# Performance work log

Measured on AMD Instinct MI355X. Metric: run time of the kernel, lower is better.

Reference implementation:

```python
import jax, jax.numpy as jnp
import numpy as np

DIM = 768
HEADS = 12
DIM_HEAD = DIM // HEADS
FACTOR = DIM_HEAD ** (-0.5)
B, T = 4, 2048


def setup_inputs() -> dict:
    key = jax.random.key(0)
    k1, k2, k3 = jax.random.split(key, 3)
    x = jax.random.normal(k1, (B, T, DIM), dtype=jnp.float32)
    # VarianceScaling-like init scale for linear weights
    W_qkv = jax.random.normal(k2, (DIM, 3 * DIM), dtype=jnp.float32) * (DIM ** -0.5)
    W_out = jax.random.normal(k3, (DIM, DIM), dtype=jnp.float32) * (DIM ** -0.5)
    return {"x": x, "W_qkv": W_qkv, "W_out": W_out}


def reference(x, W_qkv, W_out):
    b, t, _ = x.shape
    qkv = x @ W_qkv  # [b, t, 3*dim]
    # einops 'b t (d k h) -> k b h t d' with k=3, h=HEADS: d slowest, k middle, h fastest
    qkv = qkv.reshape(b, t, DIM_HEAD, 3, HEADS)
    qkv = jnp.transpose(qkv, (3, 0, 4, 1, 2))  # [3, b, h, t, d]
    q, k, v = qkv[0], qkv[1], qkv[2]
    # scaled dot-product attention, full [b,h,t,t] scores as in the original
    scores = jnp.einsum('bhid,bhjd->bhij', q, k) * FACTOR
    attn = jax.nn.softmax(scores, axis=-1)
    out = jnp.einsum('bhij,bhjd->bhid', attn, v)  # [b, h, t, d]
    # 'b h t d -> b t (h d)'
    out = jnp.transpose(out, (0, 2, 1, 3)).reshape(b, t, HEADS * DIM_HEAD)
    return out @ W_out
```

## Files before the change

kernel.cpp:

```cpp
#include <hip/hip_runtime.h>
#include <hip/hip_bf16.h>

#define DIM    768
#define HEADS  12
#define DHEAD  64
#define BATCH  4
#define SEQ    2048
#define NROW   (BATCH * SEQ)
#define QKVN   (3 * DIM)
#define FACTOR 0.125f
#define QSCALE 0.18033688011112042f

typedef __attribute__((ext_vector_type(8))) short short8;
typedef __attribute__((ext_vector_type(4))) float floatx4;

__device__ __forceinline__ floatx4 mfma16(short8 a, short8 b, floatx4 c) {
    return __builtin_amdgcn_mfma_f32_16x16x32_bf16(a, b, c, 0, 0, 0);
}

__device__ __forceinline__ short rne16(float f) {
    unsigned u = __builtin_bit_cast(unsigned, f);
    return (short)((u + 0x7fffu + ((u >> 16) & 1u)) >> 16);
}
__device__ __forceinline__ unsigned pack2(float lo, float hi) {
    unsigned ul = __builtin_bit_cast(unsigned, lo);
    unsigned uh = __builtin_bit_cast(unsigned, hi);
    ul = (ul + 0x7fffu + ((ul >> 16) & 1u)) >> 16;
    uh = (uh + 0x7fffu + ((uh >> 16) & 1u)) & 0xffff0000u;
    return ul | uh;
}

__device__ __forceinline__ int swz8(int row, int col) {
    return (row << 6) + ((((col >> 3) ^ row) & 7) << 3) + (col & 7);
}

__global__ __launch_bounds__(256) void conv_bf16(const float* __restrict__ x,
                                                 short* __restrict__ xb) {
    int g = blockIdx.x * 256 + threadIdx.x;
    float4 v = ((const float4*)x)[g];
    uint2 o;
    o.x = pack2(v.x, v.y);
    o.y = pack2(v.z, v.w);
    ((uint2*)xb)[g] = o;
}

__global__ __launch_bounds__(256) void transpose_w(const float* __restrict__ W,
                                                   short* __restrict__ Wt,
                                                   int K, int N, int permute) {
    __shared__ short T[32][33];
    int n0 = blockIdx.x * 32, k0 = blockIdx.y * 32;
    int c = threadIdx.x & 31, r0 = threadIdx.x >> 5;
    for (int r = r0; r < 32; r += 8)
        T[r][c] = rne16(W[(size_t)(k0 + r) * N + n0 + c]);
    __syncthreads();
    for (int r = r0; r < 32; r += 8) {
        int n = n0 + r;
        int np;
        if (permute) {
            int d = n / 36, rem = n - d * 36;
            int which = rem / 12, h = rem - which * 12;
            np = which * 768 + h * 64 + d;
        } else {
            np = n;
        }
        Wt[(size_t)np * K + k0 + c] = T[c][r];
    }
}

__global__ __launch_bounds__(256) void gemm_qkv(const short* __restrict__ A,
                                                const short* __restrict__ Bt,
                                                short* __restrict__ Qo,
                                                short* __restrict__ Ko,
                                                short* __restrict__ Vto) {
    __shared__ short As[128 * 64];
    __shared__ short Bs[128 * 64];
    const int tid = threadIdx.x;
    const int lane = tid & 63, wave = tid >> 6;
    const int l15 = lane & 15, quad = lane >> 4;

    const int flat = blockIdx.x;
    const int xcd = flat & 7;
    const int local = flat >> 3;
    const int mloc = local & 7, nloc = local >> 3;
    const int m0 = (xcd * 8 + mloc) * 128;
    const int n0 = nloc * 128;

    const int wm = (wave >> 1) * 64, wn = (wave & 1) * 64;

    floatx4 acc[4][4] = {};
    for (int k0 = 0; k0 < DIM; k0 += 64) {
#pragma unroll
        for (int i = 0; i < 4; ++i) {
            int idx = tid + i * 256;
            int row = idx >> 3, c = idx & 7;
            int loff = (row << 6) + (((c ^ row) & 7) << 3);
            *(uint4*)&As[loff] = *(const uint4*)&A[(size_t)(m0 + row) * DIM + k0 + c * 8];
            *(uint4*)&Bs[loff] = *(const uint4*)&Bt[(size_t)(n0 + row) * DIM + k0 + c * 8];
        }
        __syncthreads();
#pragma unroll
        for (int ks = 0; ks < 2; ++ks) {
            short8 a[4], b[4];
#pragma unroll
            for (int mt = 0; mt < 4; ++mt)
                a[mt] = *(const short8*)&As[swz8(wm + mt * 16 + l15, ks * 32 + quad * 8)];
#pragma unroll
            for (int nt = 0; nt < 4; ++nt)
                b[nt] = *(const short8*)&Bs[swz8(wn + nt * 16 + l15, ks * 32 + quad * 8)];
#pragma unroll
            for (int mt = 0; mt < 4; ++mt)
#pragma unroll
                for (int nt = 0; nt < 4; ++nt)
                    acc[mt][nt] = mfma16(a[mt], b[nt], acc[mt][nt]);
        }
        __syncthreads();
    }

    const int sn = n0 + wn;
    const int which = sn / 768;
    const int h = (sn - which * 768) >> 6;
    const int bb = (m0 + wm) >> 11;
    const int tbase = (m0 + wm) & 2047;

    if (which != 2) {
        short* dst = (which == 0) ? Qo : Ko;
        const float scale = (which == 0) ? QSCALE : 1.0f;
        const size_t rowbase = ((size_t)(bb * HEADS + h) * SEQ + tbase) * DHEAD;
#pragma unroll
        for (int mt = 0; mt < 4; ++mt)
#pragma unroll
            for (int nt = 0; nt < 4; ++nt) {
                int d = nt * 16 + l15;
#pragma unroll
                for (int r = 0; r < 4; ++r) {
                    int tl = mt * 16 + quad * 4 + r;
                    dst[rowbase + (size_t)tl * DHEAD + d] = rne16(acc[mt][nt][r] * scale);
                }
            }
    } else {
        short* vld = ((wave < 2) ? As : Bs) + (wave & 1) * 4096;
#pragma unroll
        for (int mt = 0; mt < 4; ++mt)
#pragma unroll
            for (int nt = 0; nt < 4; ++nt) {
                int d = nt * 16 + l15;
                int tl = mt * 16 + quad * 4;
                int chunk = (tl >> 3) ^ (d & 7);
                int addr = (d << 6) + (chunk << 3) + (tl & 7);
                uint2 pk;
                pk.x = pack2(acc[mt][nt][0], acc[mt][nt][1]);
                pk.y = pack2(acc[mt][nt][2], acc[mt][nt][3]);
                *(uint2*)&vld[addr] = pk;
            }
    }
    __syncthreads();
    if (which == 2) {
        short* vld = ((wave < 2) ? As : Bs) + (wave & 1) * 4096;
        const size_t vbase = ((size_t)(bb * HEADS + h) * DHEAD) * SEQ;
#pragma unroll
        for (int i = 0; i < 8; ++i) {
            int c = lane + i * 64;
            int d = c >> 3, j = c & 7;
            int addr = (d << 6) + (((j ^ (d & 7)) & 7) << 3);
            uint4 v = *(const uint4*)&vld[addr];
            *(uint4*)&Vto[vbase + (size_t)d * SEQ + tbase + j * 8] = v;
        }
    }
}

__global__ __launch_bounds__(256) void attn_mfma(const short* __restrict__ Q,
                                                 const short* __restrict__ K,
                                                 const short* __restrict__ Vt,
                                                 short* __restrict__ O) {
    __shared__ short Qs[128 * 64];
    __shared__ short Ks[64 * 64];
    __shared__ short Vs[64 * 64];
    __shared__ short Ps[4 * 32 * 64];

    const int tid = threadIdx.x;
    const int lane = tid & 63, wave = tid >> 6;
    const int l15 = lane & 15, quad = lane >> 4;
    const int bh = blockIdx.y;
    const int q0 = blockIdx.x * 128;
    const size_t base = (size_t)bh * SEQ * DHEAD;
    const int wr = wave * 32;
    short* myP = Ps + wave * (32 * 64);

#pragma unroll
    for (int i = 0; i < 4; ++i) {
        int idx = tid + i * 256;
        int row = idx >> 3, c = idx & 7;
        *(uint4*)&Qs[(row << 6) + (((c ^ row) & 7) << 3)] =
            *(const uint4*)&Q[base + (size_t)(q0 + row) * DHEAD + c * 8];
    }

    floatx4 o[2][4] = {};
    float lsum[2] = {0.f, 0.f};

    for (int j0 = 0; j0 < SEQ; j0 += 64) {
#pragma unroll
        for (int i = 0; i < 2; ++i) {
            int idx = tid + i * 256;
            int row = idx >> 3, c = idx & 7;
            int loff = (row << 6) + (((c ^ row) & 7) << 3);
            *(uint4*)&Ks[loff] = *(const uint4*)&K[base + (size_t)(j0 + row) * DHEAD + c * 8];
            *(uint4*)&Vs[loff] = *(const uint4*)&Vt[base + (size_t)row * SEQ + j0 + c * 8];
        }
        __syncthreads();

        floatx4 s[2][4] = {};
#pragma unroll
        for (int ks = 0; ks < 2; ++ks) {
            short8 kf[4], qf[2];
#pragma unroll
            for (int kt = 0; kt < 4; ++kt)
                kf[kt] = *(const short8*)&Ks[swz8(kt * 16 + l15, ks * 32 + quad * 8)];
#pragma unroll
            for (int mt = 0; mt < 2; ++mt)
                qf[mt] = *(const short8*)&Qs[swz8(wr + mt * 16 + l15, ks * 32 + quad * 8)];
#pragma unroll
            for (int mt = 0; mt < 2; ++mt)
#pragma unroll
                for (int kt = 0; kt < 4; ++kt)
                    s[mt][kt] = mfma16(kf[kt], qf[mt], s[mt][kt]);
        }

#pragma unroll
        for (int mt = 0; mt < 2; ++mt)
#pragma unroll
            for (int kt = 0; kt < 4; ++kt) {
                float p0 = __builtin_amdgcn_exp2f(s[mt][kt][0]);
                float p1 = __builtin_amdgcn_exp2f(s[mt][kt][1]);
                float p2 = __builtin_amdgcn_exp2f(s[mt][kt][2]);
                float p3 = __builtin_amdgcn_exp2f(s[mt][kt][3]);
                lsum[mt] += (p0 + p1) + (p2 + p3);
                uint2 pk;
                pk.x = pack2(p0, p1);
                pk.y = pack2(p2, p3);
                *(uint2*)&myP[swz8(mt * 16 + l15, kt * 16 + quad * 4)] = pk;
            }

#pragma unroll
        for (int ks = 0; ks < 2; ++ks) {
            short8 a[2], b[4];
#pragma unroll
            for (int mt = 0; mt < 2; ++mt)
                a[mt] = *(const short8*)&myP[swz8(mt * 16 + l15, ks * 32 + quad * 8)];
#pragma unroll
            for (int dt = 0; dt < 4; ++dt)
                b[dt] = *(const short8*)&Vs[swz8(dt * 16 + l15, ks * 32 + quad * 8)];
#pragma unroll
            for (int mt = 0; mt < 2; ++mt)
#pragma unroll
                for (int dt = 0; dt < 4; ++dt)
                    o[mt][dt] = mfma16(a[mt], b[dt], o[mt][dt]);
        }
        __syncthreads();
    }

    const int b = bh / HEADS, h = bh - b * HEADS;
#pragma unroll
    for (int mt = 0; mt < 2; ++mt) {
        float rs = lsum[mt];
        rs += __shfl_xor(rs, 16);
        rs += __shfl_xor(rs, 32);
        float invl = 1.f / rs;
#pragma unroll
        for (int r = 0; r < 4; ++r) {
            float inv = __shfl(invl, quad * 4 + r);
            int t = q0 + wr + mt * 16 + quad * 4 + r;
#pragma unroll
            for (int dt = 0; dt < 4; ++dt) {
                int d = dt * 16 + l15;
                O[((size_t)(b * SEQ + t)) * DIM + h * DHEAD + d] =
                    rne16(o[mt][dt][r] * inv);
            }
        }
    }
}

__global__ __launch_bounds__(256) void gemm_out(const short* __restrict__ A,
                                                const short* __restrict__ Bt,
                                                float* __restrict__ out) {
    __shared__ short As[128 * 64];
    __shared__ short Bs[128 * 64];
    const int tid = threadIdx.x;
    const int lane = tid & 63, wave = tid >> 6;
    const int l15 = lane & 15, quad = lane >> 4;
    const int m0 = blockIdx.y * 128, n0 = blockIdx.x * 128;
    const int wm = (wave >> 1) * 64, wn = (wave & 1) * 64;

    floatx4 acc[4][4] = {};
    for (int k0 = 0; k0 < DIM; k0 += 64) {
#pragma unroll
        for (int i = 0; i < 4; ++i) {
            int idx = tid + i * 256;
            int row = idx >> 3, c = idx & 7;
            int loff = (row << 6) + (((c ^ row) & 7) << 3);
            *(uint4*)&As[loff] = *(const uint4*)&A[(size_t)(m0 + row) * DIM + k0 + c * 8];
            *(uint4*)&Bs[loff] = *(const uint4*)&Bt[(size_t)(n0 + row) * DIM + k0 + c * 8];
        }
        __syncthreads();
#pragma unroll
        for (int ks = 0; ks < 2; ++ks) {
            short8 a[4], b[4];
#pragma unroll
            for (int mt = 0; mt < 4; ++mt)
                a[mt] = *(const short8*)&As[swz8(wm + mt * 16 + l15, ks * 32 + quad * 8)];
#pragma unroll
            for (int nt = 0; nt < 4; ++nt)
                b[nt] = *(const short8*)&Bs[swz8(wn + nt * 16 + l15, ks * 32 + quad * 8)];
#pragma unroll
            for (int mt = 0; mt < 4; ++mt)
#pragma unroll
                for (int nt = 0; nt < 4; ++nt)
                    acc[mt][nt] = mfma16(a[mt], b[nt], acc[mt][nt]);
        }
        __syncthreads();
    }

#pragma unroll
    for (int mt = 0; mt < 4; ++mt)
#pragma unroll
        for (int nt = 0; nt < 4; ++nt)
#pragma unroll
            for (int r = 0; r < 4; ++r) {
                int m = m0 + wm + mt * 16 + quad * 4 + r;
                int n = n0 + wn + nt * 16 + l15;
                out[(size_t)m * DIM + n] = acc[mt][nt][r];
            }
}

extern "C" void kernel_launch(void* const* d_in, const int* in_sizes, int n_in,
                              void* d_out, int out_size, void* d_ws, size_t ws_size,
                              hipStream_t stream) {
    const float* x    = (const float*)d_in[0];
    const float* Wqkv = (const float*)d_in[1];
    const float* Wout = (const float*)d_in[2];
    float* out = (float*)d_out;

    const size_t NE = (size_t)NROW * DIM;
    short* xb  = (short*)d_ws;
    short* Wqt = xb + NE;
    short* Wot = Wqt + (size_t)QKVN * DIM;
    short* Qw  = Wot + (size_t)DIM * DIM;
    short* Kw  = Qw + NE;
    short* Vtw = Kw + NE;

    conv_bf16<<<NE / 4 / 256, 256, 0, stream>>>(x, xb);
    transpose_w<<<dim3(QKVN / 32, DIM / 32), 256, 0, stream>>>(Wqkv, Wqt, DIM, QKVN, 1);
    transpose_w<<<dim3(DIM / 32, DIM / 32), 256, 0, stream>>>(Wout, Wot, DIM, DIM, 0);
    gemm_qkv<<<8 * 8 * 18, 256, 0, stream>>>(xb, Wqt, Qw, Kw, Vtw);
    attn_mfma<<<dim3(SEQ / 128, BATCH * HEADS), 256, 0, stream>>>(Qw, Kw, Vtw, xb);
    gemm_out<<<dim3(DIM / 128, NROW / 128), 256, 0, stream>>>(xb, Wot, out);
}
```

Baseline: 253.4 us.

## Split attention across 8 waves with register-resident Q fragments

The attention kernel now runs 512 threads per block, with each of the 8 waves owning 16 query rows instead of 32. Q fragments are loaded once into registers, so the Q tile no longer occupies LDS and its space is reused for the K/V tiles. Per-wave accumulator state is halved, which lowers register and LDS pressure and allows more waves per CU. In exchange, each K/V tile loaded into LDS is shared by more waves but is reread from LDS more often per MFMA, and barrier cost grows with the larger block.

```diff
diff --git a/kernel.cpp b/kernel.cpp
--- a/kernel.cpp
+++ b/kernel.cpp
@@ -168,14 +168,12 @@
     }
 }
 
-__global__ __launch_bounds__(256) void attn_mfma(const short* __restrict__ Q,
-                                                 const short* __restrict__ K,
-                                                 const short* __restrict__ Vt,
-                                                 short* __restrict__ O) {
-    __shared__ short Qs[128 * 64];
-    __shared__ short Ks[64 * 64];
-    __shared__ short Vs[64 * 64];
-    __shared__ short Ps[4 * 32 * 64];
+__global__ __launch_bounds__(512, 6) void attn_mfma(const short* __restrict__ Q,
+                                                    const short* __restrict__ K,
+                                                    const short* __restrict__ Vt,
+                                                    short* __restrict__ O) {
+    __shared__ short lds[128 * 64];
+    __shared__ short Ps[8 * 16 * 64];
 
     const int tid = threadIdx.x;
     const int lane = tid & 63, wave = tid >> 6;
@@ -183,98 +181,89 @@
     const int bh = blockIdx.y;
     const int q0 = blockIdx.x * 128;
     const size_t base = (size_t)bh * SEQ * DHEAD;
-    const int wr = wave * 32;
-    short* myP = Ps + wave * (32 * 64);
-
-#pragma unroll
-    for (int i = 0; i < 4; ++i) {
-        int idx = tid + i * 256;
+    const int wr = wave * 16;
+    short* myP = Ps + wave * (16 * 64);
+    short* Ks = lds;
+    short* Vs = lds + 4096;
+
+#pragma unroll
+    for (int i = 0; i < 2; ++i) {
+        int idx = tid + i * 512;
         int row = idx >> 3, c = idx & 7;
-        *(uint4*)&Qs[(row << 6) + (((c ^ row) & 7) << 3)] =
+        *(uint4*)&lds[(row << 6) + (((c ^ row) & 7) << 3)] =
             *(const uint4*)&Q[base + (size_t)(q0 + row) * DHEAD + c * 8];
     }
-
-    floatx4 o[2][4] = {};
-    float lsum[2] = {0.f, 0.f};
+    __syncthreads();
+    short8 qf[2];
+#pragma unroll
+    for (int ks = 0; ks < 2; ++ks)
+        qf[ks] = *(const short8*)&lds[swz8(wr + l15, ks * 32 + quad * 8)];
+    __syncthreads();
+
+    floatx4 o[4] = {};
+    float lsum = 0.f;
 
     for (int j0 = 0; j0 < SEQ; j0 += 64) {
-#pragma unroll
-        for (int i = 0; i < 2; ++i) {
-            int idx = tid + i * 256;
-            int row = idx >> 3, c = idx & 7;
+        {
+            int row = tid >> 3, c = tid & 7;
             int loff = (row << 6) + (((c ^ row) & 7) << 3);
             *(uint4*)&Ks[loff] = *(const uint4*)&K[base + (size_t)(j0 + row) * DHEAD + c * 8];
             *(uint4*)&Vs[loff] = *(const uint4*)&Vt[base + (size_t)row * SEQ + j0 + c * 8];
         }
         __syncthreads();
 
-        floatx4 s[2][4] = {};
+        floatx4 s[4] = {};
 #pragma unroll
         for (int ks = 0; ks < 2; ++ks) {
-            short8 kf[4], qf[2];
+            short8 kf[4];
 #pragma unroll
             for (int kt = 0; kt < 4; ++kt)
                 kf[kt] = *(const short8*)&Ks[swz8(kt * 16 + l15, ks * 32 + quad * 8)];
 #pragma unroll
-            for (int mt = 0; mt < 2; ++mt)
-                qf[mt] = *(const short8*)&Qs[swz8(wr + mt * 16 + l15, ks * 32 + quad * 8)];
-#pragma unroll
-            for (int mt = 0; mt < 2; ++mt)
-#pragma unroll
-                for (int kt = 0; kt < 4; ++kt)
-                    s[mt][kt] = mfma16(kf[kt], qf[mt], s[mt][kt]);
-        }
-
-#pragma unroll
-        for (int mt = 0; mt < 2; ++mt)
-#pragma unroll
-            for (int kt = 0; kt < 4; ++kt) {
-                float p0 = __builtin_amdgcn_exp2f(s[mt][kt][0]);
-                float p1 = __builtin_amdgcn_exp2f(s[mt][kt][1]);
-                float p2 = __builtin_amdgcn_exp2f(s[mt][kt][2]);
-                float p3 = __builtin_amdgcn_exp2f(s[mt][kt][3]);
-                lsum[mt] += (p0 + p1) + (p2 + p3);
-                uint2 pk;
-                pk.x = pack2(p0, p1);
-                pk.y = pack2(p2, p3);
-                *(uint2*)&myP[swz8(mt * 16 + l15, kt * 16 + quad * 4)] = pk;
-            }
+            for (int kt = 0; kt < 4; ++kt)
+                s[kt] = mfma16(kf[kt], qf[ks], s[kt]);
+        }
+
+#pragma unroll
+        for (int kt = 0; kt < 4; ++kt) {
+            float p0 = __builtin_amdgcn_exp2f(s[kt][0]);
+            float p1 = __builtin_amdgcn_exp2f(s[kt][1]);
+            float p2 = __builtin_amdgcn_exp2f(s[kt][2]);
+            float p3 = __builtin_amdgcn_exp2f(s[kt][3]);
+            lsum += (p0 + p1) + (p2 + p3);
+            uint2 pk;
+            pk.x = pack2(p0, p1);
+            pk.y = pack2(p2, p3);
+            *(uint2*)&myP[swz8(l15, kt * 16 + quad * 4)] = pk;
+        }
 
 #pragma unroll
         for (int ks = 0; ks < 2; ++ks) {
-            short8 a[2], b[4];
-#pragma unroll
-            for (int mt = 0; mt < 2; ++mt)
-                a[mt] = *(const short8*)&myP[swz8(mt * 16 + l15, ks * 32 + quad * 8)];
+            short8 a = *(const short8*)&myP[swz8(l15, ks * 32 + quad * 8)];
+            short8 b[4];
 #pragma unroll
             for (int dt = 0; dt < 4; ++dt)
                 b[dt] = *(const short8*)&Vs[swz8(dt * 16 + l15, ks * 32 + quad * 8)];
 #pragma unroll
-            for (int mt = 0; mt < 2; ++mt)
-#pragma unroll
-                for (int dt = 0; dt < 4; ++dt)
-                    o[mt][dt] = mfma16(a[mt], b[dt], o[mt][dt]);
+            for (int dt = 0; dt < 4; ++dt)
+                o[dt] = mfma16(a, b[dt], o[dt]);
         }
         __syncthreads();
     }
 
     const int b = bh / HEADS, h = bh - b * HEADS;
-#pragma unroll
-    for (int mt = 0; mt < 2; ++mt) {
-        float rs = lsum[mt];
-        rs += __shfl_xor(rs, 16);
-        rs += __shfl_xor(rs, 32);
-        float invl = 1.f / rs;
-#pragma unroll
-        for (int r = 0; r < 4; ++r) {
-            float inv = __shfl(invl, quad * 4 + r);
-            int t = q0 + wr + mt * 16 + quad * 4 + r;
-#pragma unroll
-            for (int dt = 0; dt < 4; ++dt) {
-                int d = dt * 16 + l15;
-                O[((size_t)(b * SEQ + t)) * DIM + h * DHEAD + d] =
-                    rne16(o[mt][dt][r] * inv);
-            }
+    float rs = lsum;
+    rs += __shfl_xor(rs, 16);
+    rs += __shfl_xor(rs, 32);
+    float invl = 1.f / rs;
+#pragma unroll
+    for (int r = 0; r < 4; ++r) {
+        float inv = __shfl(invl, quad * 4 + r);
+        int t = q0 + wr + quad * 4 + r;
+#pragma unroll
+        for (int dt = 0; dt < 4; ++dt) {
+            int d = dt * 16 + l15;
+            O[((size_t)(b * SEQ + t)) * DIM + h * DHEAD + d] = rne16(o[dt][r] * inv);
         }
     }
 }
@@ -351,6 +340,6 @@
     transpose_w<<<dim3(QKVN / 32, DIM / 32), 256, 0, stream>>>(Wqkv, Wqt, DIM, QKVN, 1);
     transpose_w<<<dim3(DIM / 32, DIM / 32), 256, 0, stream>>>(Wout, Wot, DIM, DIM, 0);
     gemm_qkv<<<8 * 8 * 18, 256, 0, stream>>>(xb, Wqt, Qw, Kw, Vtw);
-    attn_mfma<<<dim3(SEQ / 128, BATCH * HEADS), 256, 0, stream>>>(Qw, Kw, Vtw, xb);
+    attn_mfma<<<dim3(SEQ / 128, BATCH * HEADS), 512, 0, stream>>>(Qw, Kw, Vtw, xb);
     gemm_out<<<dim3(DIM / 128, NROW / 128), 256, 0, stream>>>(xb, Wot, out);
 }
```

New measurement: 237.0 us. -6.5%, faster.
